# Optimization experiments

Hardware: AMD Instinct MI355X
Metric: run time of the kernel (lower is better)

## Reference

```python
import jax, jax.numpy as jnp
import numpy as np

N_NODES = 20000
N_EDGES = 200000
D_MODEL = 128
N_HEADS = 8
N_LAYERS = 2  # num_gnn - 1 concat layers


def setup_inputs() -> dict:
    key = jax.random.key(0)
    ks = jax.random.split(key, 12)
    s = 0.05  # keep activations well-scaled across residual layers
    hd = D_MODEL // N_HEADS  # 16
    return {
        "x": jax.random.normal(ks[0], (N_NODES, D_MODEL), jnp.float32),
        "src": jax.random.randint(ks[1], (N_EDGES,), 0, N_NODES),
        "dst": jax.random.randint(ks[2], (N_EDGES,), 0, N_NODES),
        "Ws": jax.random.normal(ks[3], (N_LAYERS, D_MODEL, D_MODEL), jnp.float32) * s,
        "als": jax.random.normal(ks[4], (N_LAYERS, N_HEADS, hd), jnp.float32) * s,
        "ars": jax.random.normal(ks[5], (N_LAYERS, N_HEADS, hd), jnp.float32) * s,
        "bs": jax.random.normal(ks[6], (N_LAYERS, D_MODEL), jnp.float32) * s,
        "W_last": jax.random.normal(ks[7], (D_MODEL, N_HEADS * D_MODEL), jnp.float32) * s,
        "al_last": jax.random.normal(ks[8], (N_HEADS, D_MODEL), jnp.float32) * s,
        "ar_last": jax.random.normal(ks[9], (N_HEADS, D_MODEL), jnp.float32) * s,
        "b_last": jax.random.normal(ks[10], (N_HEADS * D_MODEL,), jnp.float32) * s,
    }


def gat_conv(h, src, dst, W, al, ar, b, num_nodes):
    """DGL GATConv (eval mode, dropout off): returns (N, H, D) head outputs."""
    H, D = al.shape
    feat = (h @ W).reshape(num_nodes, H, D)          # (N,H,D)
    el = jnp.sum(feat * al[None], axis=-1)           # (N,H) attn on src side
    er = jnp.sum(feat * ar[None], axis=-1)           # (N,H) attn on dst side
    e = jax.nn.leaky_relu(el[src] + er[dst], 0.2)    # (E,H)
    # edge softmax over incoming edges of each dst node, per head
    m = jax.ops.segment_max(e, dst, num_segments=num_nodes)  # (N,H)
    p = jnp.exp(e - m[dst])                          # (E,H)
    z = jax.ops.segment_sum(p, dst, num_segments=num_nodes)  # (N,H)
    a = p / z[dst]                                   # (E,H)
    msg = feat[src] * a[..., None]                   # (E,H,D) weighted messages
    rst = jax.ops.segment_sum(msg, dst, num_segments=num_nodes)  # (N,H,D)
    return rst + b.reshape(1, H, D)


def reference(x, src, dst, Ws, als, ars, bs, W_last, al_last, ar_last, b_last):
    N = x.shape[0]
    h = x
    for i in range(N_LAYERS):
        temp = gat_conv(h, src, dst, Ws[i], als[i], ars[i], bs[i], N)  # (N,H,hd)
        h = h + jax.nn.elu(temp.reshape(N, -1))       # concat heads, ELU, residual
    temp = gat_conv(h, src, dst, W_last, al_last, ar_last, b_last, N)  # (N,H,D)
    h = h + jnp.mean(temp, axis=1)                    # mean over heads, residual
    return h
```

## Files before the change

### kernel.cpp

```cpp
#include <hip/hip_runtime.h>
#include <math.h>

#define N_NODES 20000
#define N_EDGES 200000
#define DM 128
#define NH 8

typedef __attribute__((ext_vector_type(8))) short bf16x8;
typedef __attribute__((ext_vector_type(4))) float f32x4;

__device__ __forceinline__ unsigned short f2b(float f) {
  unsigned int u = __float_as_uint(f);
  unsigned int r = (u + 0x7FFFu + ((u >> 16) & 1u)) >> 16;
  return (unsigned short)r;
}
__device__ __forceinline__ float b2f(unsigned short s) {
  return __uint_as_float(((unsigned int)s) << 16);
}

__global__ __launch_bounds__(256) void degzero(int* __restrict__ deg) {
  int i = blockIdx.x * 256 + threadIdx.x;
  if (i < N_NODES) deg[i] = 0;
}

__global__ __launch_bounds__(256) void prep_all(
    const float* __restrict__ x, float* __restrict__ h, unsigned short* __restrict__ hb,
    const int* __restrict__ dstE, int* __restrict__ deg, int* __restrict__ rank,
    const float* __restrict__ Ws, unsigned short* __restrict__ wsz,
    const float* __restrict__ W_last, unsigned short* __restrict__ wpsz,
    const float* __restrict__ al_last, const float* __restrict__ ar_last,
    const float* __restrict__ b_last, unsigned short* __restrict__ wlrsz,
    float* __restrict__ mb) {
  int i = blockIdx.x * 256 + threadIdx.x;
  if (i < (N_NODES * DM) / 4) {
    float4 v = ((const float4*)x)[i];
    ((float4*)h)[i] = v;
    ((ushort4*)hb)[i] = make_ushort4(f2b(v.x), f2b(v.y), f2b(v.z), f2b(v.w));
  }
  if (i < N_EDGES) rank[i] = atomicAdd(&deg[dstE[i]], 1);
  if (i < 2 * 16384) {
    int layer = i >> 14;
    int r = i & 16383;
    int j = r & 7, l = (r >> 3) & 63, f = (r >> 9) & 7, ks = r >> 12;
    int k = ks * 32 + ((l >> 4) << 3) + j;
    int n = f * 16 + (l & 15);
    wsz[i] = f2b(Ws[(size_t)layer * 16384 + k * 128 + n]);
  }
  if (i < 131072) {
    int j = i & 7, l = (i >> 3) & 63, f = (i >> 9) & 7, ks = i >> 12;
    int k = ks * 32 + ((l >> 4) << 3) + j;
    int n = f * 16 + (l & 15);
    int h_ = k >> 7, ko = k & 127;
    wpsz[i] = f2b(W_last[(size_t)ko * 1024 + h_ * 128 + n] * 0.125f);
  }
  if (i < 2048) {
    int j = i & 7, l = (i >> 3) & 63, ks = i >> 9;
    int k = ks * 32 + ((l >> 4) << 3) + j;
    int n = l & 15;
    int hh = n & 7;
    const float* av = (n < 8) ? (al_last + hh * 128) : (ar_last + hh * 128);
    float s = 0.f;
    for (int d = 0; d < 128; ++d) s += W_last[(size_t)k * 1024 + hh * 128 + d] * av[d];
    wlrsz[i] = f2b(s);
  }
  if (i < 128) {
    float s = 0.f;
#pragma unroll
    for (int hh = 0; hh < 8; ++hh) s += b_last[hh * 128 + i];
    mb[i] = s * 0.125f;
  }
}

__global__ void scan_deg(const int* __restrict__ deg, int* __restrict__ off) {
  __shared__ int part[1024];
  const int tid = threadIdx.x;
  const int CHUNK = (N_NODES + 1023) / 1024;
  int base = tid * CHUNK;
  int s = 0;
  for (int i = 0; i < CHUNK; ++i) {
    int idx = base + i;
    if (idx < N_NODES) s += deg[idx];
  }
  part[tid] = s;
  __syncthreads();
  for (int ofs = 1; ofs < 1024; ofs <<= 1) {
    int v = (tid >= ofs) ? part[tid - ofs] : 0;
    __syncthreads();
    part[tid] += v;
    __syncthreads();
  }
  int run = (tid > 0) ? part[tid - 1] : 0;
  for (int i = 0; i < CHUNK; ++i) {
    int idx = base + i;
    if (idx < N_NODES) {
      off[idx] = run;
      run += deg[idx];
    }
  }
  if (tid == 0) off[N_NODES] = part[1023];
}

template <int K>
__device__ __forceinline__ void dev_gemm(int tile, const unsigned short* __restrict__ A,
                                         const unsigned short* __restrict__ Bsz,
                                         unsigned short* __restrict__ Cb,
                                         const float* __restrict__ al,
                                         const float* __restrict__ ar,
                                         float* __restrict__ elr, int lane, int wid) {
  const int wrow = wid & 1, wc = wid >> 1;
  const int r0 = tile * 32;
  const int arow = r0 + wrow * 16 + (lane & 15);
  const int kg = lane >> 4;

  f32x4 acc[4];
#pragma unroll
  for (int fi = 0; fi < 4; ++fi) acc[fi] = {0.f, 0.f, 0.f, 0.f};

  const bf16x8* Ap = (const bf16x8*)(A + (size_t)arow * K + kg * 8);
#pragma unroll 4
  for (int ks = 0; ks < K / 32; ++ks) {
    bf16x8 a = Ap[ks * 4];
#pragma unroll
    for (int fi = 0; fi < 4; ++fi) {
      int f = wc * 4 + fi;
      bf16x8 b = *(const bf16x8*)(Bsz + (((size_t)(ks * 8 + f) * 64 + lane) << 3));
      acc[fi] = __builtin_amdgcn_mfma_f32_16x16x32_bf16(a, b, acc[fi], 0, 0, 0);
    }
  }

  const int rbase = r0 + wrow * 16 + (lane >> 4) * 4;
#pragma unroll
  for (int fi = 0; fi < 4; ++fi) {
    int col = wc * 64 + fi * 16 + (lane & 15);
#pragma unroll
    for (int r = 0; r < 4; ++r) {
      Cb[(size_t)(rbase + r) * DM + col] = f2b(acc[fi][r]);
    }
  }

#pragma unroll
  for (int fi = 0; fi < 4; ++fi) {
    int hh = wc * 4 + fi;
    float alv = al[hh * 16 + (lane & 15)];
    float arv = ar[hh * 16 + (lane & 15)];
#pragma unroll
    for (int r = 0; r < 4; ++r) {
      float pl = acc[fi][r] * alv;
      float pr = acc[fi][r] * arv;
#pragma unroll
      for (int msk = 1; msk < 16; msk <<= 1) {
        pl += __shfl_xor(pl, msk, 64);
        pr += __shfl_xor(pr, msk, 64);
      }
      if ((lane & 15) == 0) {
        int row = rbase + r;
        elr[row * 16 + hh] = pl;
        elr[row * 16 + 8 + hh] = pr;
      }
    }
  }
}

__global__ __launch_bounds__(256) void gemm0_scatter(
    const unsigned short* __restrict__ A, const unsigned short* __restrict__ Bsz,
    unsigned short* __restrict__ Cb, const float* __restrict__ al,
    const float* __restrict__ ar, float* __restrict__ elr, const int* __restrict__ srcE,
    const int* __restrict__ dstE, const int* __restrict__ rank,
    const int* __restrict__ off, int* __restrict__ csr_src) {
  const int bid = blockIdx.x;
  if (bid < N_NODES / 32) {
    dev_gemm<DM>(bid, A, Bsz, Cb, al, ar, elr, threadIdx.x & 63, threadIdx.x >> 6);
  } else {
    int e = (bid - N_NODES / 32) * 256 + threadIdx.x;
    if (e < N_EDGES) {
      csr_src[off[dstE[e]] + rank[e]] = srcE[e];
    }
  }
}

template <int MODE>
__global__ __launch_bounds__(256) void fused_small(
    const int* __restrict__ off, const int* __restrict__ csr_src,
    const unsigned short* __restrict__ feat, const float* __restrict__ elr,
    const float* __restrict__ bias, float* __restrict__ h, unsigned short* __restrict__ hb,
    const unsigned short* __restrict__ wsz1, const float* __restrict__ al1,
    const float* __restrict__ ar1, unsigned short* __restrict__ feat_out,
    float* __restrict__ elr_out, const unsigned short* __restrict__ wlrsz,
    float* __restrict__ elr2_out) {
  __shared__ float a_lds[4][64];
  __shared__ int s_lds[4][8];
  __shared__ float zi_lds[4][8];
  __shared__ __align__(16) unsigned short nh_lds[4][128];
  const int wid = threadIdx.x >> 6;
  const int t = blockIdx.x * 4 + wid;
  const int lane = threadIdx.x & 63;
  const int e_loc = lane >> 3, hh = lane & 7;
  const int hg = lane >> 3;
  const int beg = off[t], end = off[t + 1];
  const float ert = elr[t * 16 + 8 + hh];

  int e = beg + e_loc;
  bool val = e < end;
  int s = val ? csr_src[e] : 0;
  float xl = val ? elr[s * 16 + hh] : 0.f;

  float z = 0.f, acc0 = 0.f, acc1 = 0.f;
  for (int base = beg; base < end; base += 8) {
    float ex = 0.f;
    if (val) {
      float xv = xl + ert;
      xv = xv > 0.f ? xv : 0.2f * xv;
      ex = __expf(xv);
    }
    a_lds[wid][lane] = ex;
    if (hh == 0) s_lds[wid][e_loc] = s;
    __builtin_amdgcn_wave_barrier();
    asm volatile("s_waitcnt lgkmcnt(0)" ::: "memory");
    z += ex;
    int en = base + 8 + e_loc;
    bool valn = en < end;
    int sn = valn ? csr_src[en] : 0;
    float xln = valn ? elr[sn * 16 + hh] : 0.f;
    int n = min(8, end - base);
    if (n == 8) {
#pragma unroll
      for (int e2 = 0; e2 < 8; ++e2) {
        int s2 = s_lds[wid][e2];
        float a = a_lds[wid][e2 * 8 + hg];
        unsigned int hv = *(const unsigned int*)&feat[(size_t)s2 * 128 + 2 * lane];
        acc0 += a * b2f((unsigned short)(hv & 0xffffu));
        acc1 += a * b2f((unsigned short)(hv >> 16));
      }
    } else {
      for (int e2 = 0; e2 < n; ++e2) {
        int s2 = s_lds[wid][e2];
        float a = a_lds[wid][e2 * 8 + hg];
        unsigned int hv = *(const unsigned int*)&feat[(size_t)s2 * 128 + 2 * lane];
        acc0 += a * b2f((unsigned short)(hv & 0xffffu));
        acc1 += a * b2f((unsigned short)(hv >> 16));
      }
    }
    __builtin_amdgcn_wave_barrier();
    s = sn;
    xl = xln;
    val = valn;
  }
  z += __shfl_xor(z, 8, 64);
  z += __shfl_xor(z, 16, 64);
  z += __shfl_xor(z, 32, 64);
  if (e_loc == 0) zi_lds[wid][hh] = (z > 0.f) ? 1.f / z : 0.f;
  __builtin_amdgcn_wave_barrier();
  asm volatile("s_waitcnt lgkmcnt(0)" ::: "memory");
  float zi = zi_lds[wid][hg];

  float2 bv = *(const float2*)&bias[2 * lane];
  float v0 = acc0 * zi + bv.x;
  float v1 = acc1 * zi + bv.y;
  v0 = v0 > 0.f ? v0 : expm1f(v0);
  v1 = v1 > 0.f ? v1 : expm1f(v1);
  size_t idx = (size_t)t * 128 + 2 * lane;
  float2 hv = *(const float2*)&h[idx];
  float nh0 = hv.x + v0;
  float nh1 = hv.y + v1;
  *(float2*)&h[idx] = make_float2(nh0, nh1);
  unsigned short b0 = f2b(nh0), b1 = f2b(nh1);
  *(ushort2*)&hb[idx] = make_ushort2(b0, b1);
  *(ushort2*)&nh_lds[wid][2 * lane] = make_ushort2(b0, b1);

  if (MODE == 1) {
    __builtin_amdgcn_wave_barrier();
    asm volatile("s_waitcnt lgkmcnt(0)" ::: "memory");
    const int kg = lane >> 4;
    f32x4 acc = {0.f, 0.f, 0.f, 0.f};
#pragma unroll
    for (int ks = 0; ks < 4; ++ks) {
      bf16x8 a = *(const bf16x8*)&nh_lds[wid][ks * 32 + kg * 8];
      bf16x8 b = *(const bf16x8*)(wlrsz + (((size_t)ks * 64 + lane) << 3));
      acc = __builtin_amdgcn_mfma_f32_16x16x32_bf16(a, b, acc, 0, 0, 0);
    }
    if (lane < 16) elr2_out[t * 16 + lane] = acc[0];
  }

  if (MODE == 0) {
    __syncthreads();
    const int t0b = blockIdx.x * 4;
    const int r16 = lane & 15;
    const int kg = lane >> 4;
    f32x4 acc2[2];
    acc2[0] = {0.f, 0.f, 0.f, 0.f};
    acc2[1] = {0.f, 0.f, 0.f, 0.f};
#pragma unroll
    for (int ks = 0; ks < 4; ++ks) {
      bf16x8 a = {0, 0, 0, 0, 0, 0, 0, 0};
      if (r16 < 4) a = *(const bf16x8*)&nh_lds[r16][ks * 32 + kg * 8];
#pragma unroll
      for (int fi = 0; fi < 2; ++fi) {
        int f = wid * 2 + fi;
        bf16x8 b = *(const bf16x8*)(wsz1 + (((size_t)(ks * 8 + f) * 64 + lane) << 3));
        acc2[fi] = __builtin_amdgcn_mfma_f32_16x16x32_bf16(a, b, acc2[fi], 0, 0, 0);
      }
    }
    const int rowl = (lane >> 4) * 4;
#pragma unroll
    for (int fi = 0; fi < 2; ++fi) {
      int f = wid * 2 + fi;
      int col = f * 16 + r16;
      float alv = al1[col];
      float arv = ar1[col];
#pragma unroll
      for (int r = 0; r < 4; ++r) {
        float v = acc2[fi][r];
        if (rowl == 0) feat_out[(size_t)(t0b + r) * 128 + col] = f2b(v);
        float pl = v * alv;
        float pr = v * arv;
#pragma unroll
        for (int msk = 1; msk < 16; msk <<= 1) {
          pl += __shfl_xor(pl, msk, 64);
          pr += __shfl_xor(pr, msk, 64);
        }
        if (r16 == 0 && rowl == 0) {
          elr_out[(t0b + r) * 16 + f] = pl;
          elr_out[(t0b + r) * 16 + 8 + f] = pr;
        }
      }
    }
  }
}

#define GT_STRIDE 1032
__global__ __launch_bounds__(1024) void agg_gemm16(
    const int* __restrict__ off, const int* __restrict__ csr_src,
    const unsigned short* __restrict__ hb, const float* __restrict__ elr,
    const unsigned short* __restrict__ wpsz, const float* __restrict__ hres,
    const float* __restrict__ mb, float* __restrict__ out) {
  __shared__ __align__(16) unsigned short gt[16][GT_STRIDE];
  __shared__ float red[8][64][4];
  __shared__ float a_lds[16][64];
  __shared__ int s_lds[16][8];
  __shared__ float zi_lds[16][8];
  const int wid = threadIdx.x >> 6;
  const int lane = threadIdx.x & 63;
  const int t0 = blockIdx.x * 16;
  const int t = t0 + wid;
  const int e_loc = lane >> 3, hh = lane & 7;

  {
    const int beg = off[t], end = off[t + 1];
    const float ert = elr[t * 16 + 8 + hh];
    int e = beg + e_loc;
    bool val = e < end;
    int s = val ? csr_src[e] : 0;
    float xl = val ? elr[s * 16 + hh] : 0.f;

    float z = 0.f;
    float accA[8], accB[8];
#pragma unroll
    for (int k = 0; k < 8; ++k) accA[k] = accB[k] = 0.f;

    for (int base = beg; base < end; base += 8) {
      float ex = 0.f;
      if (val) {
        float xv = xl + ert;
        xv = xv > 0.f ? xv : 0.2f * xv;
        ex = __expf(xv);
      }
      a_lds[wid][lane] = ex;
      if (hh == 0) s_lds[wid][e_loc] = s;
      __builtin_amdgcn_wave_barrier();
      asm volatile("s_waitcnt lgkmcnt(0)" ::: "memory");
      z += ex;
      int en = base + 8 + e_loc;
      bool valn = en < end;
      int sn = valn ? csr_src[en] : 0;
      float xln = valn ? elr[sn * 16 + hh] : 0.f;
      int n = min(8, end - base);
      if (n == 8) {
#pragma unroll
        for (int e2 = 0; e2 < 8; ++e2) {
          int s2 = s_lds[wid][e2];
          float4 pa = *(const float4*)&a_lds[wid][e2 * 8];
          float4 pb = *(const float4*)&a_lds[wid][e2 * 8 + 4];
          unsigned int hv = *(const unsigned int*)&hb[(size_t)s2 * 128 + 2 * lane];
          float h0 = b2f((unsigned short)(hv & 0xffffu));
          float h1 = b2f((unsigned short)(hv >> 16));
          accA[0] += pa.x * h0; accB[0] += pa.x * h1;
          accA[1] += pa.y * h0; accB[1] += pa.y * h1;
          accA[2] += pa.z * h0; accB[2] += pa.z * h1;
          accA[3] += pa.w * h0; accB[3] += pa.w * h1;
          accA[4] += pb.x * h0; accB[4] += pb.x * h1;
          accA[5] += pb.y * h0; accB[5] += pb.y * h1;
          accA[6] += pb.z * h0; accB[6] += pb.z * h1;
          accA[7] += pb.w * h0; accB[7] += pb.w * h1;
        }
      } else {
        for (int e2 = 0; e2 < n; ++e2) {
          int s2 = s_lds[wid][e2];
          float4 pa = *(const float4*)&a_lds[wid][e2 * 8];
          float4 pb = *(const float4*)&a_lds[wid][e2 * 8 + 4];
          unsigned int hv = *(const unsigned int*)&hb[(size_t)s2 * 128 + 2 * lane];
          float h0 = b2f((unsigned short)(hv & 0xffffu));
          float h1 = b2f((unsigned short)(hv >> 16));
          accA[0] += pa.x * h0; accB[0] += pa.x * h1;
          accA[1] += pa.y * h0; accB[1] += pa.y * h1;
          accA[2] += pa.z * h0; accB[2] += pa.z * h1;
          accA[3] += pa.w * h0; accB[3] += pa.w * h1;
          accA[4] += pb.x * h0; accB[4] += pb.x * h1;
          accA[5] += pb.y * h0; accB[5] += pb.y * h1;
          accA[6] += pb.z * h0; accB[6] += pb.z * h1;
          accA[7] += pb.w * h0; accB[7] += pb.w * h1;
        }
      }
      __builtin_amdgcn_wave_barrier();
      s = sn;
      xl = xln;
      val = valn;
    }
    z += __shfl_xor(z, 8, 64);
    z += __shfl_xor(z, 16, 64);
    z += __shfl_xor(z, 32, 64);
    if (e_loc == 0) zi_lds[wid][hh] = (z > 0.f) ? 1.f / z : 0.f;
    __builtin_amdgcn_wave_barrier();
    asm volatile("s_waitcnt lgkmcnt(0)" ::: "memory");
    float4 zia = *(const float4*)&zi_lds[wid][0];
    float4 zib = *(const float4*)&zi_lds[wid][4];
    float ziv[8] = {zia.x, zia.y, zia.z, zia.w, zib.x, zib.y, zib.z, zib.w};
#pragma unroll
    for (int h2 = 0; h2 < 8; ++h2) {
      *(ushort2*)&gt[wid][h2 * 128 + 2 * lane] =
          make_ushort2(f2b(accA[h2] * ziv[h2]), f2b(accB[h2] * ziv[h2]));
    }
  }
  __syncthreads();

  const int f = wid & 7;
  const int kh = wid >> 3;
  const int ar16 = lane & 15;
  const int kg = lane >> 4;
  f32x4 acc = {0.f, 0.f, 0.f, 0.f};
#pragma unroll 4
  for (int ksl = 0; ksl < 16; ++ksl) {
    int ks = kh * 16 + ksl;
    bf16x8 a = *(const bf16x8*)&gt[ar16][ks * 32 + kg * 8];
    bf16x8 b = *(const bf16x8*)(wpsz + (((size_t)(ks * 8 + f) * 64 + lane) << 3));
    acc = __builtin_amdgcn_mfma_f32_16x16x32_bf16(a, b, acc, 0, 0, 0);
  }
  if (kh == 1) {
    *(float4*)&red[f][lane][0] = make_float4(acc[0], acc[1], acc[2], acc[3]);
  }
  __syncthreads();
  if (kh == 0) {
    float4 p = *(const float4*)&red[f][lane][0];
    const int col = f * 16 + (lane & 15);
    const int rb = (lane >> 4) * 4;
    float r4[4] = {p.x, p.y, p.z, p.w};
#pragma unroll
    for (int r = 0; r < 4; ++r) {
      int row = t0 + rb + r;
      out[(size_t)row * 128 + col] =
          acc[r] + r4[r] + hres[(size_t)row * 128 + col] + mb[col];
    }
  }
}

extern "C" void kernel_launch(void* const* d_in, const int* in_sizes, int n_in,
                              void* d_out, int out_size, void* d_ws, size_t ws_size,
                              hipStream_t stream) {
  const float* x = (const float*)d_in[0];
  const int* src = (const int*)d_in[1];
  const int* dst = (const int*)d_in[2];
  const float* Ws = (const float*)d_in[3];
  const float* als = (const float*)d_in[4];
  const float* ars = (const float*)d_in[5];
  const float* bs = (const float*)d_in[6];
  const float* W_last = (const float*)d_in[7];
  const float* al_last = (const float*)d_in[8];
  const float* ar_last = (const float*)d_in[9];
  const float* b_last = (const float*)d_in[10];
  float* out = (float*)d_out;

  float* h = (float*)d_ws;
  float* elr0 = h + 2560000;
  float* elrB = elr0 + 320000;
  float* elr2 = elrB + 320000;
  float* mb = elr2 + 320000;
  unsigned short* hb = (unsigned short*)(mb + 128);
  unsigned short* featA = hb + 2560000;
  unsigned short* featB = featA + 2560000;
  unsigned short* wsz = featB + 2560000;
  unsigned short* wpsz = wsz + 32768;
  unsigned short* wlrsz = wpsz + 131072;
  int* deg = (int*)(wlrsz + 2048);
  int* off = deg + N_NODES;
  int* rank = off + N_NODES + 1;
  int* csr_src = rank + N_EDGES;

  const int GB = N_NODES / 32;
  const int FB = N_NODES / 4;
  const int EB = (N_EDGES + 255) / 256;

  degzero<<<(N_NODES + 255) / 256, 256, 0, stream>>>(deg);
  prep_all<<<(N_NODES * DM / 4 + 255) / 256, 256, 0, stream>>>(
      x, h, hb, dst, deg, rank, Ws, wsz, W_last, wpsz, al_last, ar_last, b_last, wlrsz, mb);
  scan_deg<<<1, 1024, 0, stream>>>(deg, off);
  gemm0_scatter<<<GB + EB, 256, 0, stream>>>(hb, wsz, featA, als, ars, elr0, src, dst,
                                             rank, off, csr_src);
  fused_small<0><<<FB, 256, 0, stream>>>(off, csr_src, featA, elr0, bs, h, hb,
                                         wsz + 16384, als + 128, ars + 128, featB, elrB,
                                         nullptr, nullptr);
  fused_small<1><<<FB, 256, 0, stream>>>(off, csr_src, featB, elrB, bs + 128, h, hb,
                                         nullptr, nullptr, nullptr, nullptr, nullptr,
                                         wlrsz, elr2);
  agg_gemm16<<<N_NODES / 16, 1024, 0, stream>>>(off, csr_src, hb, elr2, wpsz, h, mb, out);
}
```

Before: 167.6 us.

## Sort nodes by in-degree bucket to balance work across waves in blocks

Adds a counting sort of nodes by clamped in-degree inside the single-block scan kernel, producing a permutation. The aggregation kernels then process nodes in permuted order, so the waves sharing a block have similar edge counts and less time is lost waiting on the slowest wave. Outputs are scattered back through the permutation. The cost is extra serial work in the one-block scan kernel, plus scattered, less coalesced writes and reads of rows that are no longer contiguous.

New measurement: 188.1 us. +12.2%, slower.

```diff
diff --git a/kernel.cpp b/kernel.cpp
--- a/kernel.cpp
+++ b/kernel.cpp
@@ -71,8 +71,11 @@
   }
 }
 
-__global__ void scan_deg(const int* __restrict__ deg, int* __restrict__ off) {
+__global__ void scan_deg(const int* __restrict__ deg, int* __restrict__ off,
+                         int* __restrict__ perm) {
   __shared__ int part[1024];
+  __shared__ int bbase[64];
+  __shared__ int bcur[64];
   const int tid = threadIdx.x;
   const int CHUNK = (N_NODES + 1023) / 1024;
   int base = tid * CHUNK;
@@ -98,6 +101,33 @@
     }
   }
   if (tid == 0) off[N_NODES] = part[1023];
+
+  if (tid < 64) bcur[tid] = 0;
+  __syncthreads();
+  for (int i = 0; i < CHUNK; ++i) {
+    int idx = base + i;
+    if (idx < N_NODES) atomicAdd(&bcur[min(deg[idx], 63)], 1);
+  }
+  __syncthreads();
+  if (tid == 0) {
+    int r2 = 0;
+    for (int b = 0; b < 64; ++b) {
+      int c = bcur[b];
+      bbase[b] = r2;
+      r2 += c;
+    }
+  }
+  __syncthreads();
+  if (tid < 64) bcur[tid] = 0;
+  __syncthreads();
+  for (int i = 0; i < CHUNK; ++i) {
+    int idx = base + i;
+    if (idx < N_NODES) {
+      int d = min(deg[idx], 63);
+      int p = atomicAdd(&bcur[d], 1);
+      perm[bbase[d] + p] = idx;
+    }
+  }
 }
 
 template <int K>
@@ -180,24 +210,26 @@
 
 template <int MODE>
 __global__ __launch_bounds__(256) void fused_small(
-    const int* __restrict__ off, const int* __restrict__ csr_src,
-    const unsigned short* __restrict__ feat, const float* __restrict__ elr,
-    const float* __restrict__ bias, float* __restrict__ h, unsigned short* __restrict__ hb,
-    const unsigned short* __restrict__ wsz1, const float* __restrict__ al1,
-    const float* __restrict__ ar1, unsigned short* __restrict__ feat_out,
-    float* __restrict__ elr_out, const unsigned short* __restrict__ wlrsz,
-    float* __restrict__ elr2_out) {
+    const int* __restrict__ perm, const int* __restrict__ off,
+    const int* __restrict__ csr_src, const unsigned short* __restrict__ feat,
+    const float* __restrict__ elr, const float* __restrict__ bias, float* __restrict__ h,
+    unsigned short* __restrict__ hb, const unsigned short* __restrict__ wsz1,
+    const float* __restrict__ al1, const float* __restrict__ ar1,
+    unsigned short* __restrict__ feat_out, float* __restrict__ elr_out,
+    const unsigned short* __restrict__ wlrsz, float* __restrict__ elr2_out) {
   __shared__ float a_lds[4][64];
   __shared__ int s_lds[4][8];
   __shared__ float zi_lds[4][8];
   __shared__ __align__(16) unsigned short nh_lds[4][128];
+  __shared__ int pnode[4];
   const int wid = threadIdx.x >> 6;
-  const int t = blockIdx.x * 4 + wid;
+  const int t = perm[blockIdx.x * 4 + wid];
   const int lane = threadIdx.x & 63;
   const int e_loc = lane >> 3, hh = lane & 7;
   const int hg = lane >> 3;
   const int beg = off[t], end = off[t + 1];
   const float ert = elr[t * 16 + 8 + hh];
+  if (lane == 0) pnode[wid] = t;
 
   int e = beg + e_loc;
   bool val = e < end;
@@ -283,7 +315,6 @@
 
   if (MODE == 0) {
     __syncthreads();
-    const int t0b = blockIdx.x * 4;
     const int r16 = lane & 15;
     const int kg = lane >> 4;
     f32x4 acc2[2];
@@ -310,7 +341,7 @@
 #pragma unroll
       for (int r = 0; r < 4; ++r) {
         float v = acc2[fi][r];
-        if (rowl == 0) feat_out[(size_t)(t0b + r) * 128 + col] = f2b(v);
+        if (rowl == 0) feat_out[(size_t)pnode[r] * 128 + col] = f2b(v);
         float pl = v * alv;
         float pr = v * arv;
 #pragma unroll
@@ -319,8 +350,9 @@
           pr += __shfl_xor(pr, msk, 64);
         }
         if (r16 == 0 && rowl == 0) {
-          elr_out[(t0b + r) * 16 + f] = pl;
-          elr_out[(t0b + r) * 16 + 8 + f] = pr;
+          int pn = pnode[r];
+          elr_out[pn * 16 + f] = pl;
+          elr_out[pn * 16 + 8 + f] = pr;
         }
       }
     }
@@ -329,20 +361,23 @@
 
 #define GT_STRIDE 1032
 __global__ __launch_bounds__(1024) void agg_gemm16(
-    const int* __restrict__ off, const int* __restrict__ csr_src,
-    const unsigned short* __restrict__ hb, const float* __restrict__ elr,
-    const unsigned short* __restrict__ wpsz, const float* __restrict__ hres,
-    const float* __restrict__ mb, float* __restrict__ out) {
+    const int* __restrict__ perm, const int* __restrict__ off,
+    const int* __restrict__ csr_src, const unsigned short* __restrict__ hb,
+    const float* __restrict__ elr, const unsigned short* __restrict__ wpsz,
+    const float* __restrict__ hres, const float* __restrict__ mb,
+    float* __restrict__ out) {
   __shared__ __align__(16) unsigned short gt[16][GT_STRIDE];
   __shared__ float red[8][64][4];
   __shared__ float a_lds[16][64];
   __shared__ int s_lds[16][8];
   __shared__ float zi_lds[16][8];
+  __shared__ int pnode[16];
   const int wid = threadIdx.x >> 6;
   const int lane = threadIdx.x & 63;
   const int t0 = blockIdx.x * 16;
-  const int t = t0 + wid;
+  const int t = perm[t0 + wid];
   const int e_loc = lane >> 3, hh = lane & 7;
+  if (lane == 0) pnode[wid] = t;
 
   {
     const int beg = off[t], end = off[t + 1];
@@ -455,7 +490,7 @@
     float r4[4] = {p.x, p.y, p.z, p.w};
 #pragma unroll
     for (int r = 0; r < 4; ++r) {
-      int row = t0 + rb + r;
+      int row = pnode[rb + r];
       out[(size_t)row * 128 + col] =
           acc[r] + r4[r] + hres[(size_t)row * 128 + col] + mb[col];
     }
@@ -493,6 +528,7 @@
   int* off = deg + N_NODES;
   int* rank = off + N_NODES + 1;
   int* csr_src = rank + N_EDGES;
+  int* perm = csr_src + N_EDGES;
 
   const int GB = N_NODES / 32;
   const int FB = N_NODES / 4;
@@ -501,14 +537,15 @@
   degzero<<<(N_NODES + 255) / 256, 256, 0, stream>>>(deg);
   prep_all<<<(N_NODES * DM / 4 + 255) / 256, 256, 0, stream>>>(
       x, h, hb, dst, deg, rank, Ws, wsz, W_last, wpsz, al_last, ar_last, b_last, wlrsz, mb);
-  scan_deg<<<1, 1024, 0, stream>>>(deg, off);
+  scan_deg<<<1, 1024, 0, stream>>>(deg, off, perm);
   gemm0_scatter<<<GB + EB, 256, 0, stream>>>(hb, wsz, featA, als, ars, elr0, src, dst,
                                              rank, off, csr_src);
-  fused_small<0><<<FB, 256, 0, stream>>>(off, csr_src, featA, elr0, bs, h, hb,
+  fused_small<0><<<FB, 256, 0, stream>>>(perm, off, csr_src, featA, elr0, bs, h, hb,
                                          wsz + 16384, als + 128, ars + 128, featB, elrB,
                                          nullptr, nullptr);
-  fused_small<1><<<FB, 256, 0, stream>>>(off, csr_src, featB, elrB, bs + 128, h, hb,
+  fused_small<1><<<FB, 256, 0, stream>>>(perm, off, csr_src, featB, elrB, bs + 128, h, hb,
                                          nullptr, nullptr, nullptr, nullptr, nullptr,
                                          wlrsz, elr2);
-  agg_gemm16<<<N_NODES / 16, 1024, 0, stream>>>(off, csr_src, hb, elr2, wpsz, h, mb, out);
-}
+  agg_gemm16<<<N_NODES / 16, 1024, 0, stream>>>(perm, off, csr_src, hb, elr2, wpsz, h, mb,
+                                                out);
+}
```
